# Optimization experiments

Measured on AMD Instinct MI355X. Metric: run time of the kernel, lower is better.

Reference implementation:

```python
import jax, jax.numpy as jnp
import numpy as np

EXTENT = 3.0            # 'radius' arg of the model is passed as extents to ContinuousConv
SEARCH_R = EXTENT / 2.0 # Open3D fixed_radius_search uses extents/2
KS = 6                  # kernel_size [6,6,6]
N, K = 10000, 32
EPS = 1e-12
FOUR_OVER_PI = float(4.0 / np.pi)


def ball_to_cube_volume_preserving(u):
    # u: [...,3] in the unit ball -> cube [-1,1]^3 (Open3D mapping:
    # MapSphereToCylinder followed by MapCylinderToCube).
    x, y, z = u[..., 0], u[..., 1], u[..., 2]
    sq = x * x + y * y + z * z
    norm = jnp.sqrt(jnp.maximum(sq, EPS))
    rho2 = x * x + y * y
    # sphere -> cylinder (volume preserving, two regions)
    in_cone = 1.25 * z * z > rho2
    s1 = jnp.sqrt(3.0 * norm / (norm + jnp.abs(z)))
    s2 = norm / jnp.sqrt(jnp.maximum(rho2, EPS))
    s = jnp.where(in_cone, s1, s2)
    xc = x * s
    yc = y * s
    zc = jnp.where(in_cone, jnp.sign(z) * norm, 1.5 * z)
    tiny = sq < EPS
    xc = jnp.where(tiny, 0.0, xc)
    yc = jnp.where(tiny, 0.0, yc)
    zc = jnp.where(tiny, 0.0, zc)
    # cylinder -> cube (inverse concentric / Shirley-Chiu map on xy disc)
    sq_xy = xc * xc + yc * yc
    norm_xy = jnp.sqrt(jnp.maximum(sq_xy, EPS))
    x_major = jnp.abs(yc) <= jnp.abs(xc)
    xd = jnp.where(jnp.abs(xc) < EPS, 1.0, xc)
    yd = jnp.where(jnp.abs(yc) < EPS, 1.0, yc)
    tx = jnp.sign(xc) * norm_xy
    ty = jnp.sign(yc) * norm_xy
    xq = jnp.where(x_major, tx, ty * FOUR_OVER_PI * jnp.arctan(xc / yd))
    yq = jnp.where(x_major, tx * FOUR_OVER_PI * jnp.arctan(yc / xd), ty)
    tiny_xy = sq_xy < EPS
    xq = jnp.where(tiny_xy, 0.0, xq)
    yq = jnp.where(tiny_xy, 0.0, yq)
    return jnp.stack([xq, yq, zc], axis=-1)


def continuous_conv(feats, pos, nidx, nmask, W, b):
    # feats [N,Cin], pos [N,3], nidx [N,K] int32 (padded), nmask [N,K] bool
    # W [KS,KS,KS,Cin,Cout], b [Cout]
    n, k = nidx.shape
    Cin, Cout = W.shape[3], W.shape[4]
    M = KS * KS * KS
    maskf = nmask.astype(feats.dtype)
    u = (pos[nidx] - pos[:, None, :]) * (2.0 / EXTENT)          # [N,K,3], unit ball
    coords = (ball_to_cube_volume_preserving(u) + 1.0) * (0.5 * (KS - 1))  # align_corners
    i0f = jnp.floor(coords)
    frac = coords - i0f
    i0 = jnp.clip(i0f.astype(jnp.int32), 0, KS - 1)
    i1 = jnp.minimum(i0 + 1, KS - 1)
    fN = feats[nidx]                                            # [N,K,Cin]
    base = jnp.arange(n, dtype=jnp.int32)[:, None] * M          # [N,1]
    # Scatter trilinear-weighted neighbor features into per-point kernel cells:
    # A[j, cell, :] = sum_{neighbors k, corners c} w_{j,k,c} * feats[nidx[j,k]]
    A = jnp.zeros((n * M, Cin), feats.dtype)
    for cx in (0, 1):
        ix = i1[..., 0] if cx else i0[..., 0]
        wx = frac[..., 0] if cx else 1.0 - frac[..., 0]
        for cy in (0, 1):
            iy = i1[..., 1] if cy else i0[..., 1]
            wy = frac[..., 1] if cy else 1.0 - frac[..., 1]
            for cz in (0, 1):
                iz = i1[..., 2] if cz else i0[..., 2]
                wz = frac[..., 2] if cz else 1.0 - frac[..., 2]
                w = wx * wy * wz * maskf                        # [N,K]
                flat = (base + (ix * KS + iy) * KS + iz).reshape(-1)
                A = A.at[flat].add((w[..., None] * fN).reshape(n * k, Cin))
    out = jnp.einsum('nmc,mco->no', A.reshape(n, M, Cin), W.reshape(M, Cin, Cout))
    # normalize=True (Open3D default): divide by neighbor count, guarded for empty
    cnt = maskf.sum(axis=1, keepdims=True)
    out = jnp.where(cnt > 0, out / jnp.maximum(cnt, 1.0), out)
    return jax.nn.relu(out + b)                                 # use_bias + activation


def setup_inputs() -> dict:
    rng = np.random.default_rng(0)
    L = 16.0  # box side -> ~32 neighbors on average within SEARCH_R
    pos = (rng.random((N, 3)) * L).astype(np.float32)
    nidx = np.zeros((N, K), np.int32)
    nmask = np.zeros((N, K), bool)
    chunk = 512
    for s in range(0, N, chunk):
        d2 = ((pos[s:s + chunk, None, :] - pos[None, :, :]) ** 2).sum(-1)
        part = np.argpartition(d2, K, axis=1)[:, :K].astype(np.int32)
        m = np.take_along_axis(d2, part, axis=1) <= SEARCH_R * SEARCH_R
        nidx[s:s + chunk] = np.where(m, part, 0)
        nmask[s:s + chunk] = m

    def p(*shape):
        return jnp.asarray((rng.standard_normal(shape) * 0.1).astype(np.float32))

    return {
        'feats': jnp.asarray(rng.standard_normal((N, 4)).astype(np.float32)),
        'pos': jnp.asarray(pos),
        'neighbor_idx': jnp.asarray(nidx),
        'neighbor_mask': jnp.asarray(nmask),
        'W1': p(KS, KS, KS, 4, 64), 'b1': jnp.zeros((64,), jnp.float32),
        'W2': p(KS, KS, KS, 64, 64), 'b2': jnp.zeros((64,), jnp.float32),
        'W3': p(KS, KS, KS, 64, 32), 'b3': jnp.zeros((32,), jnp.float32),
        'Wfc1': p(32, 64), 'bfc1': jnp.zeros((64,), jnp.float32),
        'Wfc2': p(64, 64), 'bfc2': jnp.zeros((64,), jnp.float32),
        'Wfc3': p(64, 32), 'bfc3': jnp.zeros((32,), jnp.float32),
        'Wout': p(32, 3), 'bout': jnp.zeros((3,), jnp.float32),
    }


def reference(feats, pos, neighbor_idx, neighbor_mask, W1, b1, W2, b2, W3, b3,
              Wfc1, bfc1, Wfc2, bfc2, Wfc3, bfc3, Wout, bout):
    x = continuous_conv(feats, pos, neighbor_idx, neighbor_mask, W1, b1)
    x = continuous_conv(x, pos, neighbor_idx, neighbor_mask, W2, b2)
    x = continuous_conv(x, pos, neighbor_idx, neighbor_mask, W3, b3)
    x = jax.nn.relu(x @ Wfc1 + bfc1)
    x = jax.nn.relu(x @ Wfc2 + bfc2)
    x = jax.nn.relu(x @ Wfc3 + bfc3)
    return x @ Wout + bout
```

## Files before the change

kernel.cpp:

```cpp
#include <hip/hip_runtime.h>
#include <math.h>

#define NPTS  10000
#define KNB   32
#define NCELL 216
#define PB    16

__device__ __forceinline__ float sgnf(float v) {
    return (v > 0.0f) ? 1.0f : ((v < 0.0f) ? -1.0f : 0.0f);
}

__device__ __forceinline__ void ball_to_cube(float x, float y, float z,
                                             float& X, float& Y, float& Z) {
    const float EPSF = 1e-12f;
    const float FOPI = (float)(4.0 / 3.14159265358979323846);
    float sq   = x * x + y * y + z * z;
    float norm = sqrtf(fmaxf(sq, EPSF));
    float rho2 = x * x + y * y;
    bool in_cone = (1.25f * z * z > rho2);
    float s1 = sqrtf(3.0f * norm / (norm + fabsf(z)));
    float s2 = norm / sqrtf(fmaxf(rho2, EPSF));
    float s  = in_cone ? s1 : s2;
    float xc = x * s;
    float yc = y * s;
    float zc = in_cone ? sgnf(z) * norm : 1.5f * z;
    if (sq < EPSF) { xc = 0.0f; yc = 0.0f; zc = 0.0f; }
    float sq_xy   = xc * xc + yc * yc;
    float norm_xy = sqrtf(fmaxf(sq_xy, EPSF));
    bool x_major = (fabsf(yc) <= fabsf(xc));
    float xd = (fabsf(xc) < EPSF) ? 1.0f : xc;
    float yd = (fabsf(yc) < EPSF) ? 1.0f : yc;
    float tx = sgnf(xc) * norm_xy;
    float ty = sgnf(yc) * norm_xy;
    float xq = x_major ? tx : ty * FOPI * atanf(xc / yd);
    float yq = x_major ? tx * FOPI * atanf(yc / xd) : ty;
    if (sq_xy < EPSF) { xq = 0.0f; yq = 0.0f; }
    X = xq; Y = yq; Z = zc;
}

__global__ __launch_bounds__(256) void geom_kernel(
    const float* __restrict__ pos, const int* __restrict__ nidx,
    uint4* __restrict__ geo, float* __restrict__ cnt) {
    int t = blockIdx.x * 256 + threadIdx.x;
    if (t >= NPTS * KNB) return;
    int j = t >> 5;
    int k = t & 31;
    int nid = nidx[t];
    float px = pos[j * 3], py = pos[j * 3 + 1], pz = pos[j * 3 + 2];
    float qx = pos[nid * 3], qy = pos[nid * 3 + 1], qz = pos[nid * 3 + 2];
    float dx = __fsub_rn(px, qx), dy = __fsub_rn(py, qy), dz = __fsub_rn(pz, qz);
    float d2 = __fadd_rn(__fadd_rn(__fmul_rn(dx, dx), __fmul_rn(dy, dy)),
                         __fmul_rn(dz, dz));
    bool valid = (d2 <= 2.25f);
    if (valid && nid == 0) {
        for (int kk = 0; kk < k; ++kk) {
            if (nidx[j * KNB + kk] == 0) { valid = false; break; }
        }
    }
    uint4 g = make_uint4(0u, 0u, 0u, 0u);
    if (valid) {
        const float C = (float)(2.0 / 3.0);
        float ux = (qx - px) * C, uy = (qy - py) * C, uz = (qz - pz) * C;
        float X, Y, Z;
        ball_to_cube(ux, uy, uz, X, Y, Z);
        float cs[3] = { (X + 1.0f) * 2.5f, (Y + 1.0f) * 2.5f, (Z + 1.0f) * 2.5f };
        int i0[3], i1[3];
        float fr[3];
        #pragma unroll
        for (int d = 0; d < 3; ++d) {
            float f0 = floorf(cs[d]);
            fr[d] = cs[d] - f0;
            int a = (int)f0;
            a = min(max(a, 0), 5);
            i0[d] = a;
            i1[d] = min(a + 1, 5);
        }
        int c000 = (i0[0] * 6 + i0[1]) * 6 + i0[2];
        unsigned bits = (unsigned)c000
                      | ((unsigned)(i1[0] - i0[0]) << 8)
                      | ((unsigned)(i1[1] - i0[1]) << 9)
                      | ((unsigned)(i1[2] - i0[2]) << 10)
                      | (1u << 11)
                      | ((unsigned)nid << 12);
        g.x = __float_as_uint(fr[0]);
        g.y = __float_as_uint(fr[1]);
        g.z = __float_as_uint(fr[2]);
        g.w = bits;
        atomicAdd(&cnt[j], 1.0f);
    }
    geo[t] = g;
}

template<int CIN, int COUT>
__global__ __launch_bounds__(256) void conv_kernel(
    const float* __restrict__ feats, const float* __restrict__ W,
    const float* __restrict__ bias, const uint4* __restrict__ geo,
    const float* __restrict__ cnt, float* __restrict__ out) {
    static_assert(CIN % 4 == 0, "CIN multiple of 4");
    __shared__ uint2 contribs[4096];
    __shared__ int   bstart[4 * NCELL];
    __shared__ int   bcur[4 * NCELL];

    const int tid  = threadIdx.x;
    const int wv   = tid >> 6;
    const int lane = tid & 63;
    const int base = blockIdx.x * PB;

    for (int i = tid; i < 4 * NCELL; i += 256) bcur[i] = 0;
    __syncthreads();

    for (int pr = tid; pr < PB * KNB; pr += 256) {
        int pl = pr >> 5, k = pr & 31;
        uint4 g = geo[(base + pl) * KNB + k];
        if (g.w & 2048u) {
            int c000 = g.w & 255u;
            int dxo = (g.w & 256u)  ? 36 : 0;
            int dyo = (g.w & 512u)  ? 6  : 0;
            int dzo = (g.w & 1024u) ? 1  : 0;
            int ow  = pl >> 2;
            #pragma unroll
            for (int c = 0; c < 8; ++c) {
                int cell = c000 + ((c & 4) ? dxo : 0) + ((c & 2) ? dyo : 0)
                                + ((c & 1) ? dzo : 0);
                atomicAdd(&bcur[ow * NCELL + cell], 1);
            }
        }
    }
    __syncthreads();
    if (tid < 4) {
        int run = tid * 1024;
        for (int m = 0; m < NCELL; ++m) {
            int c = bcur[tid * NCELL + m];
            bstart[tid * NCELL + m] = run;
            run += c;
        }
    }
    __syncthreads();
    for (int i = tid; i < 4 * NCELL; i += 256) bcur[i] = bstart[i];
    __syncthreads();
    for (int pr = tid; pr < PB * KNB; pr += 256) {
        int pl = pr >> 5, k = pr & 31;
        uint4 g = geo[(base + pl) * KNB + k];
        if (g.w & 2048u) {
            float fx = __uint_as_float(g.x);
            float fy = __uint_as_float(g.y);
            float fz = __uint_as_float(g.z);
            int c000 = g.w & 255u;
            int dxo = (g.w & 256u)  ? 36 : 0;
            int dyo = (g.w & 512u)  ? 6  : 0;
            int dzo = (g.w & 1024u) ? 1  : 0;
            int nid = (g.w >> 12) & 16383u;
            int ow = pl >> 2, slot = pl & 3;
            unsigned payload = ((unsigned)slot << 14) | (unsigned)nid;
            #pragma unroll
            for (int c = 0; c < 8; ++c) {
                float wgt = ((c & 4) ? fx : 1.0f - fx)
                          * ((c & 2) ? fy : 1.0f - fy)
                          * ((c & 1) ? fz : 1.0f - fz);
                int cell = c000 + ((c & 4) ? dxo : 0) + ((c & 2) ? dyo : 0)
                                + ((c & 1) ? dzo : 0);
                int idx = atomicAdd(&bcur[ow * NCELL + cell], 1);
                contribs[idx] = make_uint2(__float_as_uint(wgt), payload);
            }
        }
    }
    __syncthreads();

    const int co = lane % COUT;
    float a0 = 0.0f, a1 = 0.0f, a2 = 0.0f, a3 = 0.0f;
    for (int m = 0; m < NCELL; ++m) {
        float wreg[CIN];
        const float* wb = W + (size_t)(m * CIN) * COUT + co;
        #pragma unroll
        for (int ci = 0; ci < CIN; ++ci) wreg[ci] = wb[ci * COUT];
        int s = bstart[wv * NCELL + m];
        int e = bcur[wv * NCELL + m];
        for (int idx = s; idx < e; ++idx) {
            uint2 cc = contribs[idx];
            float wgt = __uint_as_float(cc.x);
            int payload = __builtin_amdgcn_readfirstlane((int)cc.y);
            int nid  = payload & 16383;
            int slot = payload >> 14;
            const float* f = feats + (size_t)nid * CIN;
            float t0 = 0.0f, t1 = 0.0f, t2 = 0.0f, t3 = 0.0f;
            #pragma unroll
            for (int ci = 0; ci < CIN; ci += 4) {
                t0 = fmaf(f[ci],     wreg[ci],     t0);
                t1 = fmaf(f[ci + 1], wreg[ci + 1], t1);
                t2 = fmaf(f[ci + 2], wreg[ci + 2], t2);
                t3 = fmaf(f[ci + 3], wreg[ci + 3], t3);
            }
            float t = ((t0 + t1) + (t2 + t3)) * wgt;
            if      (slot == 0) a0 += t;
            else if (slot == 1) a1 += t;
            else if (slot == 2) a2 += t;
            else                a3 += t;
        }
        __syncthreads();
    }

    if (lane < COUT) {
        float b = bias[co];
        #pragma unroll
        for (int s2 = 0; s2 < 4; ++s2) {
            int n = base + wv * 4 + s2;
            float a = (s2 == 0) ? a0 : (s2 == 1) ? a1 : (s2 == 2) ? a2 : a3;
            float c = cnt[n];
            if (c > 0.0f) a /= fmaxf(c, 1.0f);
            a = fmaxf(a + b, 0.0f);
            out[(size_t)n * COUT + co] = a;
        }
    }
}

__global__ __launch_bounds__(64) void fc_kernel(
    const float* __restrict__ x,
    const float* __restrict__ W1, const float* __restrict__ b1,
    const float* __restrict__ W2, const float* __restrict__ b2,
    const float* __restrict__ W3, const float* __restrict__ b3,
    const float* __restrict__ W4, const float* __restrict__ b4,
    float* __restrict__ out) {
    int n = blockIdx.x;
    int lane = threadIdx.x;
    float xv = (lane < 32) ? x[(size_t)n * 32 + lane] : 0.0f;

    float t = b1[lane];
    for (int ci = 0; ci < 32; ++ci)
        t = fmaf(__shfl(xv, ci), W1[ci * 64 + lane], t);
    float h1 = fmaxf(t, 0.0f);

    t = b2[lane];
    for (int ci = 0; ci < 64; ++ci)
        t = fmaf(__shfl(h1, ci), W2[ci * 64 + lane], t);
    float h2 = fmaxf(t, 0.0f);

    int l32 = lane & 31;
    t = b3[l32];
    for (int ci = 0; ci < 64; ++ci)
        t = fmaf(__shfl(h2, ci), W3[ci * 32 + l32], t);
    float h3 = fmaxf(t, 0.0f);

    int ch = (lane < 3) ? lane : 0;
    float o = b4[ch];
    for (int ci = 0; ci < 32; ++ci)
        o = fmaf(__shfl(h3, ci), W4[ci * 3 + ch], o);
    if (lane < 3) out[(size_t)n * 3 + lane] = o;
}

extern "C" void kernel_launch(void* const* d_in, const int* in_sizes, int n_in,
                              void* d_out, int out_size, void* d_ws, size_t ws_size,
                              hipStream_t stream) {
    const float* feats = (const float*)d_in[0];
    const float* pos   = (const float*)d_in[1];
    const int*   nidx  = (const int*)d_in[2];
    const float* W1 = (const float*)d_in[4];
    const float* b1 = (const float*)d_in[5];
    const float* W2 = (const float*)d_in[6];
    const float* b2 = (const float*)d_in[7];
    const float* W3 = (const float*)d_in[8];
    const float* b3 = (const float*)d_in[9];
    const float* Wfc1 = (const float*)d_in[10];
    const float* bfc1 = (const float*)d_in[11];
    const float* Wfc2 = (const float*)d_in[12];
    const float* bfc2 = (const float*)d_in[13];
    const float* Wfc3 = (const float*)d_in[14];
    const float* bfc3 = (const float*)d_in[15];
    const float* Wout = (const float*)d_in[16];
    const float* bout = (const float*)d_in[17];

    char* ws = (char*)d_ws;
    uint4* geo = (uint4*)(ws);
    float* cnt = (float*)(ws + 5120000);
    float* x1  = (float*)(ws + 5160000);
    float* x2  = (float*)(ws + 7720000);
    float* x3  = (float*)(ws + 10280000);

    hipMemsetAsync(cnt, 0, NPTS * sizeof(float), stream);
    geom_kernel<<<(NPTS * KNB) / 256, 256, 0, stream>>>(pos, nidx, geo, cnt);

    conv_kernel<4, 64><<<NPTS / PB, 256, 0, stream>>>(feats, W1, b1, geo, cnt, x1);
    conv_kernel<64, 64><<<NPTS / PB, 256, 0, stream>>>(x1, W2, b2, geo, cnt, x2);
    conv_kernel<64, 32><<<NPTS / PB, 256, 0, stream>>>(x2, W3, b3, geo, cnt, x3);

    fc_kernel<<<NPTS, 64, 0, stream>>>(x3, Wfc1, bfc1, Wfc2, bfc2,
                                       Wfc3, bfc3, Wout, bout, (float*)d_out);
}
```

Before: 2.472 ms.

## Restructure continuous conv as gather-to-LDS plus tiled GEMM with split-K over cells

Adds a one-time sort kernel that buckets neighbor contributions by kernel cell for groups of 64 points and stores them in global memory, so all three conv layers reuse it. Each conv block now gathers interpolated features for a chunk of cells into an LDS activation tile and runs a register-blocked GEMM against double-buffered weight tiles. The cell range is split across blocks, and a combine kernel sums the partials and applies normalization, bias and ReLU. This removes the per-contribution scalar dot products and the per-block re-sorting. In exchange it adds extra kernels, a partial-sum buffer and serialized per-lane gather loops.

```diff
diff --git a/kernel.cpp b/kernel.cpp
--- a/kernel.cpp
+++ b/kernel.cpp
@@ -4,7 +4,7 @@
 #define NPTS  10000
 #define KNB   32
 #define NCELL 216
-#define PB    16
+#define NSGT  157
 
 __device__ __forceinline__ float sgnf(float v) {
     return (v > 0.0f) ? 1.0f : ((v < 0.0f) ? -1.0f : 0.0f);
@@ -91,57 +91,61 @@
     geo[t] = g;
 }
 
-template<int CIN, int COUT>
-__global__ __launch_bounds__(256) void conv_kernel(
-    const float* __restrict__ feats, const float* __restrict__ W,
-    const float* __restrict__ bias, const uint4* __restrict__ geo,
-    const float* __restrict__ cnt, float* __restrict__ out) {
-    static_assert(CIN % 4 == 0, "CIN multiple of 4");
-    __shared__ uint2 contribs[4096];
-    __shared__ int   bstart[4 * NCELL];
-    __shared__ int   bcur[4 * NCELL];
-
-    const int tid  = threadIdx.x;
-    const int wv   = tid >> 6;
-    const int lane = tid & 63;
-    const int base = blockIdx.x * PB;
-
-    for (int i = tid; i < 4 * NCELL; i += 256) bcur[i] = 0;
-    __syncthreads();
-
-    for (int pr = tid; pr < PB * KNB; pr += 256) {
-        int pl = pr >> 5, k = pr & 31;
-        uint4 g = geo[(base + pl) * KNB + k];
+__global__ __launch_bounds__(256) void sort_kernel(
+    const uint4* __restrict__ geo, uint2* __restrict__ contribs,
+    int* __restrict__ starts) {
+    __shared__ int hist[13824];
+    __shared__ int part[257];
+    const int sg = blockIdx.x, tid = threadIdx.x;
+    for (int i = tid; i < 13824; i += 256) hist[i] = 0;
+    __syncthreads();
+    const int npts = min(64, NPTS - sg * 64);
+    const int nrec = npts * KNB;
+    const uint4* gb = geo + (size_t)sg * 64 * KNB;
+    for (int r = tid; r < nrec; r += 256) {
+        uint4 g = gb[r];
         if (g.w & 2048u) {
+            int ptl = r >> 5;
             int c000 = g.w & 255u;
             int dxo = (g.w & 256u)  ? 36 : 0;
             int dyo = (g.w & 512u)  ? 6  : 0;
             int dzo = (g.w & 1024u) ? 1  : 0;
-            int ow  = pl >> 2;
             #pragma unroll
             for (int c = 0; c < 8; ++c) {
                 int cell = c000 + ((c & 4) ? dxo : 0) + ((c & 2) ? dyo : 0)
                                 + ((c & 1) ? dzo : 0);
-                atomicAdd(&bcur[ow * NCELL + cell], 1);
+                atomicAdd(&hist[cell * 64 + ptl], 1);
             }
         }
     }
     __syncthreads();
-    if (tid < 4) {
-        int run = tid * 1024;
-        for (int m = 0; m < NCELL; ++m) {
-            int c = bcur[tid * NCELL + m];
-            bstart[tid * NCELL + m] = run;
-            run += c;
-        }
-    }
-    __syncthreads();
-    for (int i = tid; i < 4 * NCELL; i += 256) bcur[i] = bstart[i];
-    __syncthreads();
-    for (int pr = tid; pr < PB * KNB; pr += 256) {
-        int pl = pr >> 5, k = pr & 31;
-        uint4 g = geo[(base + pl) * KNB + k];
+    int sum = 0;
+    for (int j = 0; j < 54; ++j) sum += hist[tid * 54 + j];
+    part[tid] = sum;
+    __syncthreads();
+    if (tid == 0) {
+        int run = 0;
+        for (int i = 0; i < 256; ++i) { int v = part[i]; part[i] = run; run += v; }
+        part[256] = run;
+    }
+    __syncthreads();
+    {
+        int run = part[tid];
+        for (int j = 0; j < 54; ++j) {
+            int i = tid * 54 + j;
+            int v = hist[i]; hist[i] = run; run += v;
+        }
+    }
+    __syncthreads();
+    for (int i = tid; i < 864; i += 256)
+        starts[sg * 865 + i] = hist[(i >> 2) * 64 + (i & 3) * 16];
+    if (tid == 0) starts[sg * 865 + 864] = part[256];
+    __syncthreads();
+    uint2* cb = contribs + (size_t)sg * 16384;
+    for (int r = tid; r < nrec; r += 256) {
+        uint4 g = gb[r];
         if (g.w & 2048u) {
+            int ptl = r >> 5;
             float fx = __uint_as_float(g.x);
             float fy = __uint_as_float(g.y);
             float fz = __uint_as_float(g.z);
@@ -150,67 +154,177 @@
             int dyo = (g.w & 512u)  ? 6  : 0;
             int dzo = (g.w & 1024u) ? 1  : 0;
             int nid = (g.w >> 12) & 16383u;
-            int ow = pl >> 2, slot = pl & 3;
-            unsigned payload = ((unsigned)slot << 14) | (unsigned)nid;
+            unsigned pay = (unsigned)nid | ((unsigned)ptl << 14);
             #pragma unroll
             for (int c = 0; c < 8; ++c) {
-                float wgt = ((c & 4) ? fx : 1.0f - fx)
-                          * ((c & 2) ? fy : 1.0f - fy)
-                          * ((c & 1) ? fz : 1.0f - fz);
+                float wgt = ((c & 4) ? fx : 1.f - fx)
+                          * ((c & 2) ? fy : 1.f - fy)
+                          * ((c & 1) ? fz : 1.f - fz);
                 int cell = c000 + ((c & 4) ? dxo : 0) + ((c & 2) ? dyo : 0)
                                 + ((c & 1) ? dzo : 0);
-                int idx = atomicAdd(&bcur[ow * NCELL + cell], 1);
-                contribs[idx] = make_uint2(__float_as_uint(wgt), payload);
+                int p = atomicAdd(&hist[cell * 64 + ptl], 1);
+                cb[p] = make_uint2(__float_as_uint(wgt), pay);
             }
         }
     }
-    __syncthreads();
-
-    const int co = lane % COUT;
-    float a0 = 0.0f, a1 = 0.0f, a2 = 0.0f, a3 = 0.0f;
-    for (int m = 0; m < NCELL; ++m) {
-        float wreg[CIN];
-        const float* wb = W + (size_t)(m * CIN) * COUT + co;
-        #pragma unroll
-        for (int ci = 0; ci < CIN; ++ci) wreg[ci] = wb[ci * COUT];
-        int s = bstart[wv * NCELL + m];
-        int e = bcur[wv * NCELL + m];
-        for (int idx = s; idx < e; ++idx) {
-            uint2 cc = contribs[idx];
-            float wgt = __uint_as_float(cc.x);
-            int payload = __builtin_amdgcn_readfirstlane((int)cc.y);
-            int nid  = payload & 16383;
-            int slot = payload >> 14;
-            const float* f = feats + (size_t)nid * CIN;
-            float t0 = 0.0f, t1 = 0.0f, t2 = 0.0f, t3 = 0.0f;
-            #pragma unroll
-            for (int ci = 0; ci < CIN; ci += 4) {
-                t0 = fmaf(f[ci],     wreg[ci],     t0);
-                t1 = fmaf(f[ci + 1], wreg[ci + 1], t1);
-                t2 = fmaf(f[ci + 2], wreg[ci + 2], t2);
-                t3 = fmaf(f[ci + 3], wreg[ci + 3], t3);
+}
+
+template<int CIN, int COUT, int CPC, int MT, int KSPLIT>
+__global__ __launch_bounds__(256, 2) void conv_kernel(
+    const float* __restrict__ feats, const float* __restrict__ W,
+    const uint2* __restrict__ contribs, const int* __restrict__ starts,
+    float* __restrict__ partial) {
+    constexpr int KC   = CPC * CIN;
+    constexpr int ASTR = KC + 4;
+    constexpr int CG   = COUT / 4;
+    constexpr int NSG  = MT / 64;
+    constexpr int NCHUNK = NCELL / CPC;
+    constexpr int NWG  = (NSG == 2) ? 2 : 1;
+    constexpr int WPT  = (KC * COUT) / 1024;
+    constexpr int RPW  = MT / 4;
+
+    __shared__ alignas(16) float Al[MT * ASTR];
+    __shared__ alignas(16) float Wl[2][KC * COUT];
+    __shared__ int Sl[NSG][868];
+
+    const int tid  = threadIdx.x;
+    const int lane = tid & 63;
+    const int wv   = tid >> 6;
+    const int cg   = tid % CG;
+    const int pg   = tid / CG;
+    const int bx   = blockIdx.x;
+    const int ks   = blockIdx.y;
+
+    for (int s = 0; s < NSG; ++s) {
+        int sg = bx * NSG + s;
+        for (int i = tid; i < 865; i += 256)
+            Sl[s][i] = (sg < NSGT) ? starts[sg * 865 + i] : 0;
+    }
+    __syncthreads();
+
+    const int c0 = NCHUNK * ks / KSPLIT;
+    const int c1 = NCHUNK * (ks + 1) / KSPLIT;
+
+    const int sgl = (NSG == 2) ? (wv >> 1) : 0;
+    const int wg0 = (NSG == 2) ? ((wv & 1) * 2) : wv;
+    const uint2* cb = contribs + (size_t)(bx * NSG + sgl) * 16384;
+
+    auto stage = [&](int c) {
+        float4 z4; z4.x = z4.y = z4.z = z4.w = 0.f;
+        float4* Az = reinterpret_cast<float4*>(Al + wv * RPW * ASTR);
+        for (int i = lane; i < RPW * (ASTR / 4); i += 64) Az[i] = z4;
+        const int cellbase = c * CPC;
+        for (int cl = 0; cl < CPC; ++cl) {
+            const int m = cellbase + cl;
+            const int key = m * 4 + wg0;
+            int s = Sl[sgl][key];
+            int e = Sl[sgl][key + NWG];
+            if (s >= e) continue;
+            const int kb = cl * CIN;
+            float vacc = 0.f;
+            int prevpt = -1;
+            int i = s;
+            while (i < e) {
+                int n2 = min(64, e - i);
+                uint2 rec = make_uint2(0u, 0u);
+                if (lane < n2) rec = cb[i + lane];
+                for (int t = 0; t < n2; ++t) {
+                    float wgt = __shfl(__uint_as_float(rec.x), t);
+                    int pay   = __shfl((int)rec.y, t);
+                    int ptl = (pay >> 14) & 63;
+                    if (ptl != prevpt) {
+                        if (prevpt >= 0 && lane < CIN)
+                            Al[(sgl * 64 + prevpt) * ASTR + kb + lane] = vacc;
+                        vacc = 0.f;
+                        prevpt = ptl;
+                    }
+                    int nid = pay & 16383;
+                    float f = (lane < CIN) ? feats[(size_t)nid * CIN + lane] : 0.f;
+                    vacc = fmaf(wgt, f, vacc);
+                }
+                i += n2;
             }
-            float t = ((t0 + t1) + (t2 + t3)) * wgt;
-            if      (slot == 0) a0 += t;
-            else if (slot == 1) a1 += t;
-            else if (slot == 2) a2 += t;
-            else                a3 += t;
+            if (prevpt >= 0 && lane < CIN)
+                Al[(sgl * 64 + prevpt) * ASTR + kb + lane] = vacc;
+        }
+    };
+
+    {
+        const float4* Wg = reinterpret_cast<const float4*>(W + (size_t)c0 * KC * COUT);
+        float4* Wd = reinterpret_cast<float4*>(Wl[0]);
+        for (int i = tid; i < KC * COUT / 4; i += 256) Wd[i] = Wg[i];
+    }
+    stage(c0);
+    __syncthreads();
+
+    float4 acc[4];
+    #pragma unroll
+    for (int p = 0; p < 4; ++p) { acc[p].x = acc[p].y = acc[p].z = acc[p].w = 0.f; }
+
+    for (int c = c0; c < c1; ++c) {
+        const int b = (c - c0) & 1;
+        float4 wpre[WPT];
+        if (c + 1 < c1) {
+            const float4* Wg = reinterpret_cast<const float4*>(W + (size_t)(c + 1) * KC * COUT);
+            #pragma unroll
+            for (int j = 0; j < WPT; ++j) wpre[j] = Wg[tid + j * 256];
+        }
+        const float* Wb = Wl[b];
+        #pragma unroll 2
+        for (int g = 0; g < KC / 4; ++g) {
+            float4 wf[4];
+            #pragma unroll
+            for (int j = 0; j < 4; ++j)
+                wf[j] = *reinterpret_cast<const float4*>(Wb + (g * 4 + j) * COUT + cg * 4);
+            float4 af[4];
+            #pragma unroll
+            for (int p = 0; p < 4; ++p)
+                af[p] = *reinterpret_cast<const float4*>(Al + (pg * 4 + p) * ASTR + g * 4);
+            #pragma unroll
+            for (int p = 0; p < 4; ++p) {
+                const float* afp = reinterpret_cast<const float*>(&af[p]);
+                #pragma unroll
+                for (int j = 0; j < 4; ++j) {
+                    float a = afp[j];
+                    acc[p].x = fmaf(a, wf[j].x, acc[p].x);
+                    acc[p].y = fmaf(a, wf[j].y, acc[p].y);
+                    acc[p].z = fmaf(a, wf[j].z, acc[p].z);
+                    acc[p].w = fmaf(a, wf[j].w, acc[p].w);
+                }
+            }
         }
         __syncthreads();
-    }
-
-    if (lane < COUT) {
-        float b = bias[co];
-        #pragma unroll
-        for (int s2 = 0; s2 < 4; ++s2) {
-            int n = base + wv * 4 + s2;
-            float a = (s2 == 0) ? a0 : (s2 == 1) ? a1 : (s2 == 2) ? a2 : a3;
-            float c = cnt[n];
-            if (c > 0.0f) a /= fmaxf(c, 1.0f);
-            a = fmaxf(a + b, 0.0f);
-            out[(size_t)n * COUT + co] = a;
-        }
-    }
+        if (c + 1 < c1) {
+            float4* Wd = reinterpret_cast<float4*>(Wl[b ^ 1]);
+            #pragma unroll
+            for (int j = 0; j < WPT; ++j) Wd[tid + j * 256] = wpre[j];
+            stage(c + 1);
+        }
+        __syncthreads();
+    }
+
+    #pragma unroll
+    for (int p = 0; p < 4; ++p) {
+        int n = bx * MT + pg * 4 + p;
+        if (n < NPTS)
+            *reinterpret_cast<float4*>(partial + ((size_t)ks * NPTS + n) * COUT + cg * 4) = acc[p];
+    }
+}
+
+template<int COUT, int KSPLIT>
+__global__ __launch_bounds__(256) void combine_kernel(
+    const float* __restrict__ partial, const float* __restrict__ cnt,
+    const float* __restrict__ bias, float* __restrict__ out) {
+    int idx = blockIdx.x * 256 + threadIdx.x;
+    if (idx >= NPTS * COUT) return;
+    int n = idx / COUT, co = idx % COUT;
+    float s = 0.f;
+    #pragma unroll
+    for (int k2 = 0; k2 < KSPLIT; ++k2)
+        s += partial[((size_t)k2 * NPTS + n) * COUT + co];
+    float c = cnt[n];
+    if (c > 0.f) s /= fmaxf(c, 1.f);
+    out[idx] = fmaxf(s + bias[co], 0.f);
 }
 
 __global__ __launch_bounds__(64) void fc_kernel(
@@ -269,18 +383,33 @@
     const float* bout = (const float*)d_in[17];
 
     char* ws = (char*)d_ws;
-    uint4* geo = (uint4*)(ws);
-    float* cnt = (float*)(ws + 5120000);
-    float* x1  = (float*)(ws + 5160000);
-    float* x2  = (float*)(ws + 7720000);
-    float* x3  = (float*)(ws + 10280000);
+    uint4* geo     = (uint4*)(ws);
+    uint2* contrib = (uint2*)(ws + 5120000);
+    float* partial = (float*)(ws + 25698304);
+    float* x1      = (float*)(ws + 30818304);
+    float* x2      = (float*)(ws + 33378304);
+    float* x3      = (float*)(ws + 35938304);
+    float* cnt     = (float*)(ws + 37218304);
+    int*   starts  = (int*)  (ws + 37258304);
 
     hipMemsetAsync(cnt, 0, NPTS * sizeof(float), stream);
     geom_kernel<<<(NPTS * KNB) / 256, 256, 0, stream>>>(pos, nidx, geo, cnt);
-
-    conv_kernel<4, 64><<<NPTS / PB, 256, 0, stream>>>(feats, W1, b1, geo, cnt, x1);
-    conv_kernel<64, 64><<<NPTS / PB, 256, 0, stream>>>(x1, W2, b2, geo, cnt, x2);
-    conv_kernel<64, 32><<<NPTS / PB, 256, 0, stream>>>(x2, W3, b3, geo, cnt, x3);
+    sort_kernel<<<NSGT, 256, 0, stream>>>(geo, contrib, starts);
+
+    conv_kernel<4, 64, 8, 64, 2><<<dim3(157, 2), 256, 0, stream>>>(
+        feats, W1, contrib, starts, partial);
+    combine_kernel<64, 2><<<(NPTS * 64 + 255) / 256, 256, 0, stream>>>(
+        partial, cnt, b1, x1);
+
+    conv_kernel<64, 64, 1, 64, 2><<<dim3(157, 2), 256, 0, stream>>>(
+        x1, W2, contrib, starts, partial);
+    combine_kernel<64, 2><<<(NPTS * 64 + 255) / 256, 256, 0, stream>>>(
+        partial, cnt, b2, x2);
+
+    conv_kernel<64, 32, 1, 128, 4><<<dim3(79, 4), 256, 0, stream>>>(
+        x2, W3, contrib, starts, partial);
+    combine_kernel<32, 4><<<(NPTS * 32 + 255) / 256, 256, 0, stream>>>(
+        partial, cnt, b3, x3);
 
     fc_kernel<<<NPTS, 64, 0, stream>>>(x3, Wfc1, bfc1, Wfc2, bfc2,
                                        Wfc3, bfc3, Wout, bout, (float*)d_out);
```

New measurement: 2.288 ms. 7.5% less time.
